# Kernel tuning notes

Hardware: AMD Instinct MI355X
Metric: run time of the kernel (lower is better)

The kernel has to match this reference:

```python
import jax, jax.numpy as jnp
import numpy as np

NEG_SLOPE = 0.2
BN_EPS = 1e-5


def _gat_conv(x, src, dst, W, a_src, a_dst, bias, heads, concat):
    # x: [N, Fin], W: [Fin, heads*C], a_src/a_dst: [heads, C]
    N = x.shape[0]
    C = W.shape[1] // heads
    h = (x @ W).reshape(N, heads, C)                       # [N, H, C]
    s_src = jnp.einsum('nhc,hc->nh', h, a_src)             # [N, H]
    s_dst = jnp.einsum('nhc,hc->nh', h, a_dst)             # [N, H]
    e = jax.nn.leaky_relu(s_src[src] + s_dst[dst], NEG_SLOPE)  # [E, H]
    # segment softmax over incoming edges of each destination node
    m = jax.ops.segment_max(e, dst, num_segments=N)
    m = jnp.where(jnp.isfinite(m), m, 0.0)
    ex = jnp.exp(e - m[dst])
    denom = jax.ops.segment_sum(ex, dst, num_segments=N)
    alpha = ex / (denom[dst] + 1e-16)                      # [E, H]
    out = jax.ops.segment_sum(alpha[:, :, None] * h[src], dst, num_segments=N)  # [N,H,C]
    if concat:
        out = out.reshape(N, heads * C)
    else:
        out = out.mean(axis=1)
    return out + bias


def setup_inputs() -> dict:
    key = jax.random.key(0)
    ks = jax.random.split(key, 12)
    N, E, Fin, Ch, H, Fout = 50000, 800000, 128, 32, 4, 2
    Fhid = Ch * H  # 128
    x = jax.random.normal(ks[0], (N, Fin), dtype=jnp.float32)
    edge_index = jax.random.randint(ks[1], (2, E), 0, N, dtype=jnp.int64)
    def glorot(k, shape):
        fan = shape[0] + shape[-1]
        return jax.random.normal(k, shape, dtype=jnp.float32) * jnp.sqrt(2.0 / fan)
    return {
        'x': x,
        'edge_index': edge_index,
        'W1': glorot(ks[2], (Fin, Fhid)),
        'att_src1': glorot(ks[3], (H, Ch)),
        'att_dst1': glorot(ks[4], (H, Ch)),
        'b1': jnp.zeros((Fhid,), jnp.float32),
        'gamma': jnp.ones((Fhid,), jnp.float32),
        'beta': jnp.zeros((Fhid,), jnp.float32),
        'W2': glorot(ks[5], (Fhid, Fout)),
        'att_src2': glorot(ks[6], (1, Fout)),
        'att_dst2': glorot(ks[7], (1, Fout)),
        'b2': jnp.zeros((Fout,), jnp.float32),
    }


def reference(x, edge_index, W1, att_src1, att_dst1, b1, gamma, beta,
              W2, att_src2, att_dst2, b2):
    N = x.shape[0]
    # PyG GATConv adds self-loops by default
    loops = jnp.arange(N, dtype=edge_index.dtype)
    src = jnp.concatenate([edge_index[0], loops])
    dst = jnp.concatenate([edge_index[1], loops])
    h = _gat_conv(x, src, dst, W1, att_src1, att_dst1, b1, heads=4, concat=True)
    # BatchNorm1d (batch statistics, train-mode math)
    mu = h.mean(axis=0)
    var = h.var(axis=0)
    h = (h - mu) * jax.lax.rsqrt(var + BN_EPS) * gamma + beta
    h = jax.nn.elu(h)
    # dropout = 0 (eval)
    out = _gat_conv(h, src, dst, W2, att_src2, att_dst2, b2, heads=1, concat=False)
    return out
```

## Files before the change

kernel.cpp:

```cpp
#include <hip/hip_runtime.h>
#include <hip/hip_bf16.h>
#include <math.h>

#define FH 128
#define NEG_SLOPE 0.2f
#define BN_EPS 1e-5f

__global__ __launch_bounds__(256) void k_gemm1(
    const float* __restrict__ x, const float* __restrict__ W,
    const float* __restrict__ asrc, const float* __restrict__ adst,
    float* __restrict__ h1, float* __restrict__ ssrc, float* __restrict__ sdst,
    int N)
{
    __shared__ float xs[64][132];
    __shared__ float Ws[128][64];
    const int t = threadIdx.x;
    const int row0 = blockIdx.x * 64;
    const int col0 = blockIdx.y * 64;

    #pragma unroll
    for (int i = 0; i < 8; ++i) {
        int f = (i * 256 + t) * 4;
        int r = f >> 7, c = f & 127;
        float4 v = make_float4(0.f, 0.f, 0.f, 0.f);
        if (row0 + r < N) v = *(const float4*)(x + (size_t)(row0 + r) * FH + c);
        xs[r][c] = v.x; xs[r][c + 1] = v.y; xs[r][c + 2] = v.z; xs[r][c + 3] = v.w;
    }
    #pragma unroll
    for (int i = 0; i < 8; ++i) {
        int f = (i * 256 + t) * 4;
        int k = f >> 6, c = f & 63;
        *(float4*)&Ws[k][c] = *(const float4*)(W + (size_t)k * FH + col0 + c);
    }
    __syncthreads();

    const int r  = t >> 3;
    const int cq = (t & 7) * 8;
    float accA[8] = {0,0,0,0,0,0,0,0};
    float accB[8] = {0,0,0,0,0,0,0,0};
    #pragma unroll 4
    for (int k = 0; k < 128; ++k) {
        float xa = xs[r][k];
        float xb = xs[r + 32][k];
        float4 w0 = *(const float4*)&Ws[k][cq];
        float4 w1 = *(const float4*)&Ws[k][cq + 4];
        accA[0] = fmaf(xa, w0.x, accA[0]); accA[1] = fmaf(xa, w0.y, accA[1]);
        accA[2] = fmaf(xa, w0.z, accA[2]); accA[3] = fmaf(xa, w0.w, accA[3]);
        accA[4] = fmaf(xa, w1.x, accA[4]); accA[5] = fmaf(xa, w1.y, accA[5]);
        accA[6] = fmaf(xa, w1.z, accA[6]); accA[7] = fmaf(xa, w1.w, accA[7]);
        accB[0] = fmaf(xb, w0.x, accB[0]); accB[1] = fmaf(xb, w0.y, accB[1]);
        accB[2] = fmaf(xb, w0.z, accB[2]); accB[3] = fmaf(xb, w0.w, accB[3]);
        accB[4] = fmaf(xb, w1.x, accB[4]); accB[5] = fmaf(xb, w1.y, accB[5]);
        accB[6] = fmaf(xb, w1.z, accB[6]); accB[7] = fmaf(xb, w1.w, accB[7]);
    }

    const int hg = (col0 >> 5) + (cq >> 5);
    const int cl = cq & 31;
    float4 as0 = *(const float4*)(asrc + hg * 32 + cl);
    float4 as1 = *(const float4*)(asrc + hg * 32 + cl + 4);
    float4 ad0 = *(const float4*)(adst + hg * 32 + cl);
    float4 ad1 = *(const float4*)(adst + hg * 32 + cl + 4);
    float sA = accA[0]*as0.x + accA[1]*as0.y + accA[2]*as0.z + accA[3]*as0.w
             + accA[4]*as1.x + accA[5]*as1.y + accA[6]*as1.z + accA[7]*as1.w;
    float dA = accA[0]*ad0.x + accA[1]*ad0.y + accA[2]*ad0.z + accA[3]*ad0.w
             + accA[4]*ad1.x + accA[5]*ad1.y + accA[6]*ad1.z + accA[7]*ad1.w;
    float sB = accB[0]*as0.x + accB[1]*as0.y + accB[2]*as0.z + accB[3]*as0.w
             + accB[4]*as1.x + accB[5]*as1.y + accB[6]*as1.z + accB[7]*as1.w;
    float dB = accB[0]*ad0.x + accB[1]*ad0.y + accB[2]*ad0.z + accB[3]*ad0.w
             + accB[4]*ad1.x + accB[5]*ad1.y + accB[6]*ad1.z + accB[7]*ad1.w;
    sA += __shfl_xor(sA, 1, 64); sA += __shfl_xor(sA, 2, 64);
    dA += __shfl_xor(dA, 1, 64); dA += __shfl_xor(dA, 2, 64);
    sB += __shfl_xor(sB, 1, 64); sB += __shfl_xor(sB, 2, 64);
    dB += __shfl_xor(dB, 1, 64); dB += __shfl_xor(dB, 2, 64);

    int ra = row0 + r, rb = row0 + r + 32;
    if (ra < N) {
        float* p = h1 + (size_t)ra * FH + col0 + cq;
        *(float4*)p       = make_float4(accA[0], accA[1], accA[2], accA[3]);
        *(float4*)(p + 4) = make_float4(accA[4], accA[5], accA[6], accA[7]);
        if ((t & 3) == 0) { ssrc[ra * 4 + hg] = sA; sdst[ra * 4 + hg] = dA; }
    }
    if (rb < N) {
        float* p = h1 + (size_t)rb * FH + col0 + cq;
        *(float4*)p       = make_float4(accB[0], accB[1], accB[2], accB[3]);
        *(float4*)(p + 4) = make_float4(accB[4], accB[5], accB[6], accB[7]);
        if ((t & 3) == 0) { ssrc[rb * 4 + hg] = sB; sdst[rb * 4 + hg] = dB; }
    }
}

__global__ void k_count(const int* __restrict__ ei, int E, int N, int* __restrict__ deg) {
    int i = blockIdx.x * blockDim.x + threadIdx.x;
    if (i >= E + N) return;
    int d = (i < E) ? ei[E + i] : (i - E);
    atomicAdd(&deg[d], 1);
}

__global__ __launch_bounds__(1024) void k_scan1(const int* __restrict__ deg,
                                                int* __restrict__ rowptr,
                                                int* __restrict__ blksum, int N) {
    int t = threadIdx.x;
    int i = blockIdx.x * 1024 + t;
    int v = (i < N) ? deg[i] : 0;
    int lane = t & 63, w = t >> 6;
    int incl = v;
    #pragma unroll
    for (int off = 1; off < 64; off <<= 1) {
        int tmp = __shfl_up(incl, off, 64);
        if (lane >= off) incl += tmp;
    }
    __shared__ int wsum[16];
    if (lane == 63) wsum[w] = incl;
    __syncthreads();
    if (t == 0) {
        int s = 0;
        for (int k = 0; k < 16; ++k) { int x = wsum[k]; wsum[k] = s; s += x; }
    }
    __syncthreads();
    int excl = incl - v + wsum[w];
    if (i < N) rowptr[i] = excl;
    if (t == 1023) blksum[blockIdx.x] = excl + v;
}

__global__ __launch_bounds__(1024) void k_scan2(const int* __restrict__ blksum,
                                                int* __restrict__ blkoff, int nblk) {
    int t = threadIdx.x;
    int v = (t < nblk) ? blksum[t] : 0;
    int lane = t & 63, w = t >> 6;
    int incl = v;
    #pragma unroll
    for (int off = 1; off < 64; off <<= 1) {
        int tmp = __shfl_up(incl, off, 64);
        if (lane >= off) incl += tmp;
    }
    __shared__ int wsum[16];
    if (lane == 63) wsum[w] = incl;
    __syncthreads();
    if (t == 0) {
        int s = 0;
        for (int k = 0; k < 16; ++k) { int x = wsum[k]; wsum[k] = s; s += x; }
    }
    __syncthreads();
    int excl = incl - v + wsum[w];
    if (t < nblk) blkoff[t] = excl;
    if (t == nblk - 1) blkoff[nblk] = excl + v;
}

__global__ void k_scan3(int* __restrict__ rowptr, const int* __restrict__ blkoff, int N) {
    int i = blockIdx.x * blockDim.x + threadIdx.x;
    if (i > N) return;
    if (i == N) rowptr[N] = blkoff[(N + 1023) >> 10];
    else        rowptr[i] += blkoff[i >> 10];
}

__global__ void k_fill(const int* __restrict__ ei, int E, int N,
                       const int* __restrict__ rowptr, int* __restrict__ deg,
                       int* __restrict__ csr) {
    int i = blockIdx.x * blockDim.x + threadIdx.x;
    if (i >= E + N) return;
    int s, d;
    if (i < E) { s = ei[i]; d = ei[E + i]; }
    else       { s = i - E; d = i - E; }
    int pos = atomicSub(&deg[d], 1) - 1;
    csr[rowptr[d] + pos] = s;
}

__global__ __launch_bounds__(256) void k_agg1(
    const int* __restrict__ rowptr, const int* __restrict__ csr,
    const float* __restrict__ h1, const float* __restrict__ ssrc,
    const float* __restrict__ sdst, const float* __restrict__ b1,
    float* __restrict__ out, int N)
{
    int n = (blockIdx.x * blockDim.x + threadIdx.x) >> 6;
    int lane = threadIdx.x & 63;
    if (n >= N) return;
    int start = rowptr[n];
    int dcnt  = rowptr[n + 1] - start;

    float4 sd4 = *(const float4*)(sdst + n * 4);
    float mx = -3e38f, my = -3e38f, mz = -3e38f, mw = -3e38f;
    float lx = 0.f, ly = 0.f, lz = 0.f, lw = 0.f;
    for (int j = lane; j < dcnt; j += 64) {
        int s = csr[start + j];
        float4 sv = *(const float4*)(ssrc + s * 4);
        float ex = sv.x + sd4.x; ex = ex > 0.f ? ex : NEG_SLOPE * ex;
        float ey = sv.y + sd4.y; ey = ey > 0.f ? ey : NEG_SLOPE * ey;
        float ez = sv.z + sd4.z; ez = ez > 0.f ? ez : NEG_SLOPE * ez;
        float ew = sv.w + sd4.w; ew = ew > 0.f ? ew : NEG_SLOPE * ew;
        float nm;
        nm = fmaxf(mx, ex); lx = lx * __expf(mx - nm) + __expf(ex - nm); mx = nm;
        nm = fmaxf(my, ey); ly = ly * __expf(my - nm) + __expf(ey - nm); my = nm;
        nm = fmaxf(mz, ez); lz = lz * __expf(mz - nm) + __expf(ez - nm); mz = nm;
        nm = fmaxf(mw, ew); lw = lw * __expf(mw - nm) + __expf(ew - nm); mw = nm;
    }
    float pmx = mx, pmy = my, pmz = mz, pmw = mw;
    #pragma unroll
    for (int off = 32; off; off >>= 1) {
        mx = fmaxf(mx, __shfl_xor(mx, off, 64));
        my = fmaxf(my, __shfl_xor(my, off, 64));
        mz = fmaxf(mz, __shfl_xor(mz, off, 64));
        mw = fmaxf(mw, __shfl_xor(mw, off, 64));
    }
    lx *= __expf(pmx - mx); ly *= __expf(pmy - my);
    lz *= __expf(pmz - mz); lw *= __expf(pmw - mw);
    #pragma unroll
    for (int off = 32; off; off >>= 1) {
        lx += __shfl_xor(lx, off, 64);
        ly += __shfl_xor(ly, off, 64);
        lz += __shfl_xor(lz, off, 64);
        lw += __shfl_xor(lw, off, 64);
    }

    int h = lane >> 4;
    float Mh  = h == 0 ? mx : h == 1 ? my : h == 2 ? mz : mw;
    float Lh  = h == 0 ? lx : h == 1 ? ly : h == 2 ? lz : lw;
    float sdh = h == 0 ? sd4.x : h == 1 ? sd4.y : h == 2 ? sd4.z : sd4.w;
    float invl = 1.f / (Lh + 1e-16f);

    float ax = 0.f, ay = 0.f;
    const float2* h1v = (const float2*)h1;
    #pragma unroll 4
    for (int j = 0; j < dcnt; ++j) {
        int s = csr[start + j];
        float e = ssrc[s * 4 + h] + sdh;
        e = e > 0.f ? e : NEG_SLOPE * e;
        float p = __expf(e - Mh);
        float2 v = h1v[(size_t)s * 64 + lane];
        ax = fmaf(p, v.x, ax);
        ay = fmaf(p, v.y, ay);
    }
    float2 o;
    o.x = fmaf(ax, invl, b1[2 * lane]);
    o.y = fmaf(ay, invl, b1[2 * lane + 1]);
    ((float2*)out)[(size_t)n * 64 + lane] = o;
}

__global__ __launch_bounds__(256) void k_bnstat(const float4* __restrict__ hb4,
                                                float* __restrict__ bnsum,
                                                float* __restrict__ bnsq, int N) {
    __shared__ float rs[8][128];
    __shared__ float rq[8][128];
    int t = threadIdx.x;
    int rg = t >> 5, c4 = t & 31;
    float sx = 0, sy = 0, sz = 0, sw = 0, qx = 0, qy = 0, qz = 0, qw = 0;
    for (int r = blockIdx.x * 8 + rg; r < N; r += gridDim.x * 8) {
        float4 v = hb4[(size_t)r * 32 + c4];
        sx += v.x; sy += v.y; sz += v.z; sw += v.w;
        qx = fmaf(v.x, v.x, qx); qy = fmaf(v.y, v.y, qy);
        qz = fmaf(v.z, v.z, qz); qw = fmaf(v.w, v.w, qw);
    }
    int c = c4 * 4;
    rs[rg][c] = sx; rs[rg][c+1] = sy; rs[rg][c+2] = sz; rs[rg][c+3] = sw;
    rq[rg][c] = qx; rq[rg][c+1] = qy; rq[rg][c+2] = qz; rq[rg][c+3] = qw;
    __syncthreads();
    for (int k = 4; k; k >>= 1) {
        if (rg < k) {
            rs[rg][c]   += rs[rg+k][c];   rs[rg][c+1] += rs[rg+k][c+1];
            rs[rg][c+2] += rs[rg+k][c+2]; rs[rg][c+3] += rs[rg+k][c+3];
            rq[rg][c]   += rq[rg+k][c];   rq[rg][c+1] += rq[rg+k][c+1];
            rq[rg][c+2] += rq[rg+k][c+2]; rq[rg][c+3] += rq[rg+k][c+3];
        }
        __syncthreads();
    }
    if (t < 32) {
        int cc = t * 4;
        atomicAdd(&bnsum[cc],   rs[0][cc]);   atomicAdd(&bnsum[cc+1], rs[0][cc+1]);
        atomicAdd(&bnsum[cc+2], rs[0][cc+2]); atomicAdd(&bnsum[cc+3], rs[0][cc+3]);
        atomicAdd(&bnsq[cc],    rq[0][cc]);   atomicAdd(&bnsq[cc+1],  rq[0][cc+1]);
        atomicAdd(&bnsq[cc+2],  rq[0][cc+2]); atomicAdd(&bnsq[cc+3],  rq[0][cc+3]);
    }
}

__global__ __launch_bounds__(256) void k_bn2(const float4* __restrict__ hb4,
                                             const float* __restrict__ bnsum,
                                             const float* __restrict__ bnsq,
                                             const float* __restrict__ gamma,
                                             const float* __restrict__ beta,
                                             const float* __restrict__ W2,
                                             const float* __restrict__ as2,
                                             const float* __restrict__ ad2,
                                             float4* __restrict__ node2,
                                             int N, float invN) {
    int t = threadIdx.x;
    int rl = t >> 5, c4 = t & 31;
    int r = blockIdx.x * 8 + rl;
    if (r >= N) return;
    int c = c4 * 4;
    float4 s4 = *(const float4*)(bnsum + c);
    float4 q4 = *(const float4*)(bnsq + c);
    float4 g4 = *(const float4*)(gamma + c);
    float4 be4 = *(const float4*)(beta + c);
    float mu0 = s4.x * invN, mu1 = s4.y * invN, mu2 = s4.z * invN, mu3 = s4.w * invN;
    float sc0 = rsqrtf(q4.x * invN - mu0 * mu0 + BN_EPS) * g4.x;
    float sc1 = rsqrtf(q4.y * invN - mu1 * mu1 + BN_EPS) * g4.y;
    float sc2 = rsqrtf(q4.z * invN - mu2 * mu2 + BN_EPS) * g4.z;
    float sc3 = rsqrtf(q4.w * invN - mu3 * mu3 + BN_EPS) * g4.w;
    float sh0 = be4.x - mu0 * sc0, sh1 = be4.y - mu1 * sc1;
    float sh2 = be4.z - mu2 * sc2, sh3 = be4.w - mu3 * sc3;

    float4 v = hb4[(size_t)r * 32 + c4];
    float t0 = fmaf(v.x, sc0, sh0);
    float t1 = fmaf(v.y, sc1, sh1);
    float t2 = fmaf(v.z, sc2, sh2);
    float t3 = fmaf(v.w, sc3, sh3);
    t0 = t0 > 0.f ? t0 : expm1f(t0);
    t1 = t1 > 0.f ? t1 : expm1f(t1);
    t2 = t2 > 0.f ? t2 : expm1f(t2);
    t3 = t3 > 0.f ? t3 : expm1f(t3);
    float d0 = t0 * W2[c * 2]       + t1 * W2[(c + 1) * 2]
             + t2 * W2[(c + 2) * 2] + t3 * W2[(c + 3) * 2];
    float d1 = t0 * W2[c * 2 + 1]       + t1 * W2[(c + 1) * 2 + 1]
             + t2 * W2[(c + 2) * 2 + 1] + t3 * W2[(c + 3) * 2 + 1];
    #pragma unroll
    for (int off = 16; off; off >>= 1) {
        d0 += __shfl_xor(d0, off, 64);
        d1 += __shfl_xor(d1, off, 64);
    }
    if (c4 == 0) {
        float4 o;
        o.x = d0; o.y = d1;
        o.z = d0 * as2[0] + d1 * as2[1];
        o.w = d0 * ad2[0] + d1 * ad2[1];
        node2[r] = o;
    }
}

__global__ __launch_bounds__(256) void k_agg2(const int* __restrict__ rowptr,
                                              const int* __restrict__ csr,
                                              const float4* __restrict__ node2,
                                              const float* __restrict__ b2,
                                              float* __restrict__ out, int N) {
    int gid = blockIdx.x * blockDim.x + threadIdx.x;
    int n = gid >> 4;
    int ln = gid & 15;
    if (n >= N) return;
    int start = rowptr[n];
    int dcnt  = rowptr[n + 1] - start;
    float sdv = node2[n].w;
    float m = -3e38f, l = 0.f, a0 = 0.f, a1 = 0.f;
    for (int j = ln; j < dcnt; j += 16) {
        int s = csr[start + j];
        float4 hv = node2[s];
        float e = hv.z + sdv;
        e = e > 0.f ? e : NEG_SLOPE * e;
        float nm = fmaxf(m, e);
        float sc = __expf(m - nm);
        float p  = __expf(e - nm);
        a0 = a0 * sc + p * hv.x;
        a1 = a1 * sc + p * hv.y;
        l  = l * sc + p;
        m  = nm;
    }
    #pragma unroll
    for (int off = 8; off; off >>= 1) {
        float mo  = __shfl_xor(m, off, 64);
        float lo  = __shfl_xor(l, off, 64);
        float a0o = __shfl_xor(a0, off, 64);
        float a1o = __shfl_xor(a1, off, 64);
        float nm = fmaxf(m, mo);
        float sc = __expf(m - nm), so = __expf(mo - nm);
        l  = l * sc + lo * so;
        a0 = a0 * sc + a0o * so;
        a1 = a1 * sc + a1o * so;
        m  = nm;
    }
    if (ln == 0) {
        float inv = 1.f / (l + 1e-16f);
        float2 o;
        o.x = fmaf(a0, inv, b2[0]);
        o.y = fmaf(a1, inv, b2[1]);
        ((float2*)out)[n] = o;
    }
}

extern "C" void kernel_launch(void* const* d_in, const int* in_sizes, int n_in,
                              void* d_out, int out_size, void* d_ws, size_t ws_size,
                              hipStream_t stream) {
    const int N = in_sizes[0] / FH;
    const int E = in_sizes[1] / 2;
    const int Etot = E + N;
    const int nblk = (N + 1023) >> 10;

    const float* x     = (const float*)d_in[0];
    const int*   ei    = (const int*)d_in[1];
    const float* W1    = (const float*)d_in[2];
    const float* asrc1 = (const float*)d_in[3];
    const float* adst1 = (const float*)d_in[4];
    const float* b1    = (const float*)d_in[5];
    const float* gamma = (const float*)d_in[6];
    const float* beta  = (const float*)d_in[7];
    const float* W2    = (const float*)d_in[8];
    const float* as2   = (const float*)d_in[9];
    const float* ad2   = (const float*)d_in[10];
    const float* b2    = (const float*)d_in[11];
    float* out = (float*)d_out;

    char* ws = (char*)d_ws;
    size_t off = 0;
    auto nxt = [&](size_t bytes) {
        size_t o = off;
        off += (bytes + 255) & ~(size_t)255;
        return o;
    };
    float* h1      = (float*)(ws + nxt((size_t)N * FH * 4));
    float* hb      = (float*)(ws + nxt((size_t)N * FH * 4));
    float* ssrc1   = (float*)(ws + nxt((size_t)N * 4 * 4));
    float* sdst1   = (float*)(ws + nxt((size_t)N * 4 * 4));
    float* node2   = (float*)(ws + nxt((size_t)N * 4 * 4));
    size_t zoff0   = off;
    int*   deg     = (int*)(ws + nxt((size_t)N * 4));
    float* bnsum   = (float*)(ws + nxt(128 * 4));
    float* bnsq    = (float*)(ws + nxt(128 * 4));
    size_t zbytes  = off - zoff0;
    int*   rowptr  = (int*)(ws + nxt((size_t)(N + 1) * 4));
    int*   csr     = (int*)(ws + nxt((size_t)Etot * 4));
    int*   blksum  = (int*)(ws + nxt((size_t)nblk * 4));
    int*   blkoff  = (int*)(ws + nxt((size_t)(nblk + 1) * 4));

    hipMemsetAsync(ws + zoff0, 0, zbytes, stream);

    dim3 g1((N + 63) / 64, 2);
    k_gemm1<<<g1, 256, 0, stream>>>(x, W1, asrc1, adst1, h1, ssrc1, sdst1, N);
    k_count<<<(Etot + 255) / 256, 256, 0, stream>>>(ei, E, N, deg);
    k_scan1<<<nblk, 1024, 0, stream>>>(deg, rowptr, blksum, N);
    k_scan2<<<1, 1024, 0, stream>>>(blksum, blkoff, nblk);
    k_scan3<<<(N + 256) / 256, 256, 0, stream>>>(rowptr, blkoff, N);
    k_fill<<<(Etot + 255) / 256, 256, 0, stream>>>(ei, E, N, rowptr, deg, csr);
    k_agg1<<<(N + 3) / 4, 256, 0, stream>>>(rowptr, csr, h1, ssrc1, sdst1, b1, hb, N);
    k_bnstat<<<512, 256, 0, stream>>>((const float4*)hb, bnsum, bnsq, N);
    k_bn2<<<(N + 7) / 8, 256, 0, stream>>>((const float4*)hb, bnsum, bnsq, gamma, beta,
                                           W2, as2, ad2, (float4*)node2, N,
                                           1.0f / (float)N);
    k_agg2<<<(N * 16 + 255) / 256, 256, 0, stream>>>(rowptr, csr, (const float4*)node2,
                                                     b2, out, N);
}
```

Measured before the change: 350.6 us.

## Store layer-1 features in fp16 and fold softmax denominator into aggregation pass

The first GEMM now writes the projected node features as half precision, which halves the bytes gathered per edge in the layer-1 aggregation. The aggregation's first pass now only computes the per-head max, and the softmax denominator is accumulated alongside the weighted sum in the second pass, so the first pass no longer evaluates exponentials. Leaky-ReLU is rewritten as an fmax. The cost is reduced precision of the gathered features, which may affect accuracy against the fp32 reference.

Measured after the change: 335.0 us. -4.5%, faster.

```diff
diff --git a/kernel.cpp b/kernel.cpp
--- a/kernel.cpp
+++ b/kernel.cpp
@@ -1,5 +1,6 @@
 #include <hip/hip_runtime.h>
 #include <hip/hip_bf16.h>
+#include <hip/hip_fp16.h>
 #include <math.h>
 
 #define FH 128
@@ -9,7 +10,7 @@
 __global__ __launch_bounds__(256) void k_gemm1(
     const float* __restrict__ x, const float* __restrict__ W,
     const float* __restrict__ asrc, const float* __restrict__ adst,
-    float* __restrict__ h1, float* __restrict__ ssrc, float* __restrict__ sdst,
+    __half* __restrict__ h1h, float* __restrict__ ssrc, float* __restrict__ sdst,
     int N)
 {
     __shared__ float xs[64][132];
@@ -75,15 +76,21 @@
 
     int ra = row0 + r, rb = row0 + r + 32;
     if (ra < N) {
-        float* p = h1 + (size_t)ra * FH + col0 + cq;
-        *(float4*)p       = make_float4(accA[0], accA[1], accA[2], accA[3]);
-        *(float4*)(p + 4) = make_float4(accA[4], accA[5], accA[6], accA[7]);
+        __half2 ph[4];
+        ph[0] = __floats2half2_rn(accA[0], accA[1]);
+        ph[1] = __floats2half2_rn(accA[2], accA[3]);
+        ph[2] = __floats2half2_rn(accA[4], accA[5]);
+        ph[3] = __floats2half2_rn(accA[6], accA[7]);
+        *(uint4*)(h1h + (size_t)ra * FH + col0 + cq) = *(uint4*)ph;
         if ((t & 3) == 0) { ssrc[ra * 4 + hg] = sA; sdst[ra * 4 + hg] = dA; }
     }
     if (rb < N) {
-        float* p = h1 + (size_t)rb * FH + col0 + cq;
-        *(float4*)p       = make_float4(accB[0], accB[1], accB[2], accB[3]);
-        *(float4*)(p + 4) = make_float4(accB[4], accB[5], accB[6], accB[7]);
+        __half2 ph[4];
+        ph[0] = __floats2half2_rn(accB[0], accB[1]);
+        ph[1] = __floats2half2_rn(accB[2], accB[3]);
+        ph[2] = __floats2half2_rn(accB[4], accB[5]);
+        ph[3] = __floats2half2_rn(accB[6], accB[7]);
+        *(uint4*)(h1h + (size_t)rb * FH + col0 + cq) = *(uint4*)ph;
         if ((t & 3) == 0) { ssrc[rb * 4 + hg] = sB; sdst[rb * 4 + hg] = dB; }
     }
 }
@@ -166,7 +173,7 @@
 
 __global__ __launch_bounds__(256) void k_agg1(
     const int* __restrict__ rowptr, const int* __restrict__ csr,
-    const float* __restrict__ h1, const float* __restrict__ ssrc,
+    const __half* __restrict__ h1h, const float* __restrict__ ssrc,
     const float* __restrict__ sdst, const float* __restrict__ b1,
     float* __restrict__ out, int N)
 {
@@ -178,21 +185,16 @@
 
     float4 sd4 = *(const float4*)(sdst + n * 4);
     float mx = -3e38f, my = -3e38f, mz = -3e38f, mw = -3e38f;
-    float lx = 0.f, ly = 0.f, lz = 0.f, lw = 0.f;
     for (int j = lane; j < dcnt; j += 64) {
         int s = csr[start + j];
         float4 sv = *(const float4*)(ssrc + s * 4);
-        float ex = sv.x + sd4.x; ex = ex > 0.f ? ex : NEG_SLOPE * ex;
-        float ey = sv.y + sd4.y; ey = ey > 0.f ? ey : NEG_SLOPE * ey;
-        float ez = sv.z + sd4.z; ez = ez > 0.f ? ez : NEG_SLOPE * ez;
-        float ew = sv.w + sd4.w; ew = ew > 0.f ? ew : NEG_SLOPE * ew;
-        float nm;
-        nm = fmaxf(mx, ex); lx = lx * __expf(mx - nm) + __expf(ex - nm); mx = nm;
-        nm = fmaxf(my, ey); ly = ly * __expf(my - nm) + __expf(ey - nm); my = nm;
-        nm = fmaxf(mz, ez); lz = lz * __expf(mz - nm) + __expf(ez - nm); mz = nm;
-        nm = fmaxf(mw, ew); lw = lw * __expf(mw - nm) + __expf(ew - nm); mw = nm;
-    }
-    float pmx = mx, pmy = my, pmz = mz, pmw = mw;
+        float ex = sv.x + sd4.x; ex = fmaxf(ex, NEG_SLOPE * ex);
+        float ey = sv.y + sd4.y; ey = fmaxf(ey, NEG_SLOPE * ey);
+        float ez = sv.z + sd4.z; ez = fmaxf(ez, NEG_SLOPE * ez);
+        float ew = sv.w + sd4.w; ew = fmaxf(ew, NEG_SLOPE * ew);
+        mx = fmaxf(mx, ex); my = fmaxf(my, ey);
+        mz = fmaxf(mz, ez); mw = fmaxf(mw, ew);
+    }
     #pragma unroll
     for (int off = 32; off; off >>= 1) {
         mx = fmaxf(mx, __shfl_xor(mx, off, 64));
@@ -200,38 +202,30 @@
         mz = fmaxf(mz, __shfl_xor(mz, off, 64));
         mw = fmaxf(mw, __shfl_xor(mw, off, 64));
     }
-    lx *= __expf(pmx - mx); ly *= __expf(pmy - my);
-    lz *= __expf(pmz - mz); lw *= __expf(pmw - mw);
-    #pragma unroll
-    for (int off = 32; off; off >>= 1) {
-        lx += __shfl_xor(lx, off, 64);
-        ly += __shfl_xor(ly, off, 64);
-        lz += __shfl_xor(lz, off, 64);
-        lw += __shfl_xor(lw, off, 64);
-    }
 
     int h = lane >> 4;
     float Mh  = h == 0 ? mx : h == 1 ? my : h == 2 ? mz : mw;
-    float Lh  = h == 0 ? lx : h == 1 ? ly : h == 2 ? lz : lw;
     float sdh = h == 0 ? sd4.x : h == 1 ? sd4.y : h == 2 ? sd4.z : sd4.w;
-    float invl = 1.f / (Lh + 1e-16f);
-
-    float ax = 0.f, ay = 0.f;
-    const float2* h1v = (const float2*)h1;
+
+    float ax = 0.f, ay = 0.f, l = 0.f;
+    const __half2* h1v = (const __half2*)h1h;
     #pragma unroll 4
     for (int j = 0; j < dcnt; ++j) {
         int s = csr[start + j];
         float e = ssrc[s * 4 + h] + sdh;
-        e = e > 0.f ? e : NEG_SLOPE * e;
+        e = fmaxf(e, NEG_SLOPE * e);
         float p = __expf(e - Mh);
-        float2 v = h1v[(size_t)s * 64 + lane];
+        l += p;
+        float2 v = __half22float2(h1v[((size_t)s << 6) + lane]);
         ax = fmaf(p, v.x, ax);
         ay = fmaf(p, v.y, ay);
     }
+    float inv = 1.f / (l + 1e-16f);
+    float2 b1v = ((const float2*)b1)[lane];
     float2 o;
-    o.x = fmaf(ax, invl, b1[2 * lane]);
-    o.y = fmaf(ay, invl, b1[2 * lane + 1]);
-    ((float2*)out)[(size_t)n * 64 + lane] = o;
+    o.x = fmaf(ax, inv, b1v.x);
+    o.y = fmaf(ay, inv, b1v.y);
+    ((float2*)out)[((size_t)n << 6) + lane] = o;
 }
 
 __global__ __launch_bounds__(256) void k_bnstat(const float4* __restrict__ hb4,
@@ -341,7 +335,7 @@
         int s = csr[start + j];
         float4 hv = node2[s];
         float e = hv.z + sdv;
-        e = e > 0.f ? e : NEG_SLOPE * e;
+        e = fmaxf(e, NEG_SLOPE * e);
         float nm = fmaxf(m, e);
         float sc = __expf(m - nm);
         float p  = __expf(e - nm);
@@ -401,7 +395,7 @@
         off += (bytes + 255) & ~(size_t)255;
         return o;
     };
-    float* h1      = (float*)(ws + nxt((size_t)N * FH * 4));
+    __half* h1h    = (__half*)(ws + nxt((size_t)N * FH * 2));
     float* hb      = (float*)(ws + nxt((size_t)N * FH * 4));
     float* ssrc1   = (float*)(ws + nxt((size_t)N * 4 * 4));
     float* sdst1   = (float*)(ws + nxt((size_t)N * 4 * 4));
@@ -419,13 +413,13 @@
     hipMemsetAsync(ws + zoff0, 0, zbytes, stream);
 
     dim3 g1((N + 63) / 64, 2);
-    k_gemm1<<<g1, 256, 0, stream>>>(x, W1, asrc1, adst1, h1, ssrc1, sdst1, N);
+    k_gemm1<<<g1, 256, 0, stream>>>(x, W1, asrc1, adst1, h1h, ssrc1, sdst1, N);
     k_count<<<(Etot + 255) / 256, 256, 0, stream>>>(ei, E, N, deg);
     k_scan1<<<nblk, 1024, 0, stream>>>(deg, rowptr, blksum, N);
     k_scan2<<<1, 1024, 0, stream>>>(blksum, blkoff, nblk);
     k_scan3<<<(N + 256) / 256, 256, 0, stream>>>(rowptr, blkoff, N);
     k_fill<<<(Etot + 255) / 256, 256, 0, stream>>>(ei, E, N, rowptr, deg, csr);
-    k_agg1<<<(N + 3) / 4, 256, 0, stream>>>(rowptr, csr, h1, ssrc1, sdst1, b1, hb, N);
+    k_agg1<<<(N + 3) / 4, 256, 0, stream>>>(rowptr, csr, h1h, ssrc1, sdst1, b1, hb, N);
     k_bnstat<<<512, 256, 0, stream>>>((const float4*)hb, bnsum, bnsq, N);
     k_bn2<<<(N + 7) / 8, 256, 0, stream>>>((const float4*)hb, bnsum, bnsq, gamma, beta,
                                            W2, as2, ad2, (float4*)node2, N,
```
